# Optimization experiments

Measured on AMD Instinct MI355X. Metric: run time of the kernel, lower is better.

## Reference

```python
import jax, jax.numpy as jnp
import numpy as np

B, S, L = 2, 2048, 2048
H, KVH, D = 16, 4, 128
HID = H * D
EPS = 1e-6
SCALE = 1.0 / np.sqrt(D)


def rmsnorm(x, w, eps=EPS):
    # normalize over last dim (head_size), fp32 math
    xf = x.astype(jnp.float32)
    var = jnp.mean(xf * xf, axis=-1, keepdims=True)
    return (xf * jax.lax.rsqrt(var + eps)).astype(x.dtype) * w


def setup_inputs() -> dict:
    key = jax.random.key(0)
    ks = jax.random.split(key, 5)
    s = 1.0 / np.sqrt(HID)
    return {
        "x": jax.random.normal(ks[0], (B, S, HID), jnp.float32),
        "c": jax.random.normal(ks[1], (B, L, HID), jnp.float32),
        "wq": jax.random.normal(ks[2], (HID, H * D), jnp.float32) * s,
        "wkv": jax.random.normal(ks[3], (HID, KVH * D * 2), jnp.float32) * s,
        "wo": jax.random.normal(ks[4], (H * D, HID), jnp.float32) * s,
        "norm_q_w": jnp.ones((D,), jnp.float32),
        "norm_k_w": jnp.ones((D,), jnp.float32),
    }


def reference(x, c, wq, wkv, wo, norm_q_w, norm_k_w):
    bs, seq_len, _ = x.shape
    c_len = c.shape[1]
    n_rep = H // KVH
    # Q projection + per-head RMSNorm
    xq = (x @ wq).reshape(bs, seq_len, H, D)
    xq = rmsnorm(xq, norm_q_w)
    # packed KV projection: view(..., kvh, hd, 2), unbind last dim
    ckv = (c @ wkv).reshape(bs, c_len, KVH, D, 2)
    ck, cv = ckv[..., 0], ckv[..., 1]
    ck = rmsnorm(ck, norm_k_w)
    # GQA repeat_kv (repeat_interleave over head dim)
    ck = jnp.repeat(ck, n_rep, axis=2)  # [b, L, H, D]
    cv = jnp.repeat(cv, n_rep, axis=2)
    # SDPA cross-attention, softmax in fp32
    scores = jnp.einsum("bqhd,bkhd->bhqk", xq, ck) * SCALE
    attn = jax.nn.softmax(scores.astype(jnp.float32), axis=-1).astype(xq.dtype)
    out = jnp.einsum("bhqk,bkhd->bqhd", attn, cv)
    out = out.reshape(bs, seq_len, H * D)
    return out @ wo
```

## Files before the change

### kernel.cpp

```cpp
#include <hip/hip_runtime.h>

#define B_ 2
#define S_ 2048
#define L_ 2048
#define H_ 16
#define KVH_ 4
#define D_ 128
#define HID_ 2048
#define EPS_ 1e-6f

typedef unsigned short u16;
typedef unsigned int u32;
typedef __bf16 bf16x8 __attribute__((ext_vector_type(8)));
typedef float f32x4 __attribute__((ext_vector_type(4)));
typedef unsigned u32x2v __attribute__((ext_vector_type(2)));
typedef unsigned u32x4v __attribute__((ext_vector_type(4)));

__device__ __forceinline__ float bf2f(u32 u) {
  union { u32 i; float f; } x; x.i = u << 16; return x.f;
}
__device__ __forceinline__ u16 f2bf(float f) {
  union { float f; u32 i; } x; x.f = f;
  return (u16)((x.i + 0x7fffu + ((x.i >> 16) & 1u)) >> 16);
}
__device__ __forceinline__ u32 pack_bf16(float a, float b) {
#if __has_builtin(__builtin_amdgcn_cvt_pk_bf16_f32)
  typedef __bf16 bf16x2 __attribute__((ext_vector_type(2)));
  union { bf16x2 v; u32 u; } c;
  c.v = __builtin_amdgcn_cvt_pk_bf16_f32(a, b);
  return c.u;
#else
  return (u32)f2bf(a) | ((u32)f2bf(b) << 16);
#endif
}
__device__ __forceinline__ void gl2lds16(const u16* g, u16* l) {
  __builtin_amdgcn_global_load_lds(
      (const __attribute__((address_space(1))) u32*)g,
      (__attribute__((address_space(3))) u32*)l, 16, 0, 0);
}

#if __has_builtin(__builtin_amdgcn_permlane32_swap) && __has_builtin(__builtin_amdgcn_permlane16_swap)
#define HAS_PLS 1
#else
#define HAS_PLS 0
#endif

__device__ __forceinline__ u32x4v ctoa(u32 xa, u32 xb, u32 ya, u32 yb,
                                       int quad, int l15) {
  u32x4v f;
#if HAS_PLS
  u32x2v t1 = __builtin_amdgcn_permlane32_swap(xa, ya, false, false);
  u32x2v t2 = __builtin_amdgcn_permlane16_swap(t1.x, t1.y, false, false);
  u32x2v t3 = __builtin_amdgcn_permlane32_swap(xb, yb, false, false);
  u32x2v t4 = __builtin_amdgcn_permlane16_swap(t3.x, t3.y, false, false);
  f.x = t2.x; f.y = t4.x; f.z = t2.y; f.w = t4.y;
#else
  int a0 = (((2 * quad) & 3) * 16 + l15) << 2;
  int a1 = (((2 * quad + 1) & 3) * 16 + l15) << 2;
  u32 xa0 = __builtin_amdgcn_ds_bpermute(a0, xa), ya0 = __builtin_amdgcn_ds_bpermute(a0, ya);
  u32 xb0 = __builtin_amdgcn_ds_bpermute(a0, xb), yb0 = __builtin_amdgcn_ds_bpermute(a0, yb);
  u32 xa1 = __builtin_amdgcn_ds_bpermute(a1, xa), ya1 = __builtin_amdgcn_ds_bpermute(a1, ya);
  u32 xb1 = __builtin_amdgcn_ds_bpermute(a1, xb), yb1 = __builtin_amdgcn_ds_bpermute(a1, yb);
  bool hi = quad >= 2;
  f.x = hi ? ya0 : xa0; f.y = hi ? yb0 : xb0;
  f.z = hi ? ya1 : xa1; f.w = hi ? yb1 : xb1;
#endif
  return f;
}

__global__ __launch_bounds__(256) void cvt_bf16(const float* __restrict__ in,
                                                u16* __restrict__ out, int n4) {
  int i = blockIdx.x * 256 + threadIdx.x;
  if (i >= n4) return;
  float4 v = ((const float4*)in)[i];
  uint2 o;
  o.x = pack_bf16(v.x, v.y);
  o.y = pack_bf16(v.z, v.w);
  ((uint2*)out)[i] = o;
}

__global__ __launch_bounds__(256) void transp_bf16(const float* __restrict__ A,
                                                   u16* __restrict__ At, int R, int C) {
  __shared__ float t[64][65];
  int c0 = blockIdx.x * 64, r0 = blockIdx.y * 64;
  int tx = threadIdx.x & 63, ty = threadIdx.x >> 6;
  for (int i = ty; i < 64; i += 4)
    t[i][tx] = A[(size_t)(r0 + i) * C + c0 + tx];
  __syncthreads();
  for (int i = ty; i < 64; i += 4)
    At[(size_t)(c0 + i) * R + r0 + tx] = f2bf(t[tx][i]);
}

__device__ __forceinline__ void store_out(u16* p, float v) { *p = f2bf(v); }
__device__ __forceinline__ void store_out(float* p, float v) { *p = v; }

template <typename OutT>
__global__ __launch_bounds__(256, 2) void gemm_bt(const u16* __restrict__ A,
                                                  const u16* __restrict__ Bt,
                                                  OutT* __restrict__ C,
                                                  int M, int N, int K) {
  __shared__ u16 sA[128 * 32];
  __shared__ u16 sB[128 * 32];
  const int tid = threadIdx.x;
  const int wave = tid >> 6, lane = tid & 63;
  const int quad = lane >> 4, l15 = lane & 15;
  const int m0 = blockIdx.x * 128, n0 = blockIdx.y * 128;
  const int wm = (wave >> 1) * 64, wn = (wave & 1) * 64;
  const u16* aP = A + (size_t)m0 * K;
  const u16* bP = Bt + (size_t)n0 * K;
  const int sr = lane >> 2;
  const int sc = (lane & 3) * 8;
  const int r0 = wave * 32, r1 = wave * 32 + 16;

  f32x4 acc[4][4];
  for (int i = 0; i < 4; i++)
    for (int j = 0; j < 4; j++)
      for (int r = 0; r < 4; r++) acc[i][j][r] = 0.0f;

  for (int k0 = 0; k0 < K; k0 += 32) {
    gl2lds16(aP + (size_t)(r0 + sr) * K + k0 + sc, &sA[r0 * 32]);
    gl2lds16(aP + (size_t)(r1 + sr) * K + k0 + sc, &sA[r1 * 32]);
    gl2lds16(bP + (size_t)(r0 + sr) * K + k0 + sc, &sB[r0 * 32]);
    gl2lds16(bP + (size_t)(r1 + sr) * K + k0 + sc, &sB[r1 * 32]);
    __syncthreads();
    bf16x8 afrag[4], bfrag[4];
    for (int i = 0; i < 4; i++)
      afrag[i] = *(const bf16x8*)&sA[(wm + i * 16 + l15) * 32 + quad * 8];
    for (int j = 0; j < 4; j++)
      bfrag[j] = *(const bf16x8*)&sB[(wn + j * 16 + l15) * 32 + quad * 8];
    for (int i = 0; i < 4; i++)
      for (int j = 0; j < 4; j++)
        acc[i][j] = __builtin_amdgcn_mfma_f32_16x16x32_bf16(afrag[i], bfrag[j], acc[i][j], 0, 0, 0);
    __syncthreads();
  }
  for (int i = 0; i < 4; i++)
    for (int j = 0; j < 4; j++) {
      int row = m0 + wm + i * 16 + quad * 4;
      int col = n0 + wn + j * 16 + l15;
      for (int r = 0; r < 4; r++)
        store_out(&C[(size_t)(row + r) * N + col], acc[i][j][r]);
    }
}

__global__ __launch_bounds__(256) void knorm_deint(const u16* __restrict__ CKV,
                                                   const float* __restrict__ w,
                                                   u16* __restrict__ K,
                                                   u16* __restrict__ Vt) {
  __shared__ u16 vbuf[128][66];
  const int tid = threadIdx.x, wave = tid >> 6, lane = tid & 63;
  const int l0 = blockIdx.x * 64, kvh = blockIdx.y, b = blockIdx.z;
  for (int it = 0; it < 16; it++) {
    int ll = wave * 16 + it;
    int row = b * L_ + l0 + ll;
    const u16* src = CKV + (size_t)row * 1024 + kvh * 256;
    u32 p0 = *(const u32*)&src[lane * 2];
    u32 p1 = *(const u32*)&src[(lane + 64) * 2];
    float k0 = bf2f(p0 & 0xffff), v0 = bf2f(p0 >> 16);
    float k1 = bf2f(p1 & 0xffff), v1 = bf2f(p1 >> 16);
    float ss = k0 * k0 + k1 * k1;
    for (int off = 1; off < 64; off <<= 1) ss += __shfl_xor(ss, off);
    float sc = rsqrtf(ss * (1.0f / 128.0f) + EPS_);
    size_t kb = (((size_t)b * KVH_ + kvh) * L_ + l0 + ll) * D_;
    K[kb + lane] = f2bf(k0 * sc * w[lane]);
    K[kb + lane + 64] = f2bf(k1 * sc * w[lane + 64]);
    vbuf[lane][ll] = f2bf(v0);
    vbuf[lane + 64][ll] = f2bf(v1);
  }
  __syncthreads();
  for (int it = tid; it < 128 * 32; it += 256) {
    int d = it >> 5, cc = (it & 31) * 2;
    u32 pk = (u32)vbuf[d][cc] | ((u32)vbuf[d][cc + 1] << 16);
    *(u32*)&Vt[(((size_t)b * KVH_ + kvh) * D_ + d) * L_ + l0 + cc] = pk;
  }
}

__global__ __launch_bounds__(256, 2) void attn(const u16* __restrict__ XQ,
                                               const float* __restrict__ nw,
                                               const u16* __restrict__ K,
                                               const u16* __restrict__ Vt,
                                               u16* __restrict__ AO) {
  __shared__ u16 sk[4][128 * 32];
  __shared__ u16 sv[4][128 * 32];
  const int tid = threadIdx.x, wave = tid >> 6, lane = tid & 63;
  const int quad = lane >> 4, l15 = lane & 15;
  const int qt = blockIdx.x, h = blockIdx.y, b = blockIdx.z;
  const int kvh = h >> 2;
  const int s0 = qt * 128, wr0 = wave * 32;

  bf16x8 qf[2][4];
  {
    const float cexp = 0.12753102331322172f;
    const u16* qrow = XQ + (size_t)(b * S_ + s0 + wr0 + l15) * HID_ + h * D_;
    for (int i = 0; i < 2; i++) {
      const u16* qr = qrow + (size_t)i * 16 * HID_;
      float vals[4][8];
      float ss = 0.0f;
      for (int kc = 0; kc < 4; kc++) {
        uint4 u = *(const uint4*)&qr[kc * 32 + quad * 8];
        u32 uu[4] = {u.x, u.y, u.z, u.w};
        for (int e = 0; e < 4; e++) {
          float lo = bf2f(uu[e] & 0xffff), hi = bf2f(uu[e] >> 16);
          vals[kc][2 * e] = lo;
          vals[kc][2 * e + 1] = hi;
          ss += lo * lo + hi * hi;
        }
      }
      ss += __shfl_xor(ss, 16);
      ss += __shfl_xor(ss, 32);
      float scale = rsqrtf(ss * (1.0f / 128.0f) + EPS_) * cexp;
      for (int kc = 0; kc < 4; kc++) {
        float4 w0 = *(const float4*)&nw[kc * 32 + quad * 8];
        float4 w1 = *(const float4*)&nw[kc * 32 + quad * 8 + 4];
        union { u32x4v u; bf16x8 v; } q;
        q.u.x = pack_bf16(vals[kc][0] * scale * w0.x, vals[kc][1] * scale * w0.y);
        q.u.y = pack_bf16(vals[kc][2] * scale * w0.z, vals[kc][3] * scale * w0.w);
        q.u.z = pack_bf16(vals[kc][4] * scale * w1.x, vals[kc][5] * scale * w1.y);
        q.u.w = pack_bf16(vals[kc][6] * scale * w1.z, vals[kc][7] * scale * w1.w);
        qf[i][kc] = q.v;
      }
    }
  }

  float psum[2] = {0.0f, 0.0f};
  f32x4 o[2][8];
  for (int i = 0; i < 2; i++)
    for (int n = 0; n < 8; n++)
      for (int r = 0; r < 4; r++) o[i][n][r] = 0.0f;

  const u16* kbase = K + ((size_t)(b * KVH_ + kvh) * L_) * D_;
  const u16* vbase = Vt + ((size_t)(b * KVH_ + kvh) * D_) * L_;
  const int srow = lane >> 2;
  const int scol = ((lane & 3) ^ ((lane >> 3) & 3)) * 8;
  const int swq = (quad ^ ((l15 >> 1) & 3)) * 8;

  for (int l0 = 0; l0 < L_; l0 += 128) {
    const u16* kb = kbase + (size_t)l0 * D_ + wave * 32;
    for (int is = 0; is < 8; is++)
      gl2lds16(kb + (size_t)(is * 16 + srow) * D_ + scol, &sk[wave][is * 16 * 32]);
    const u16* vb = vbase + l0 + wave * 32;
    for (int is = 0; is < 8; is++)
      gl2lds16(vb + (size_t)(is * 16 + srow) * L_ + scol, &sv[wave][is * 16 * 32]);
    __syncthreads();

    for (int cc = 0; cc < 4; cc++) {
      f32x4 sacc[2][2];
      for (int jj = 0; jj < 2; jj++)
        for (int i = 0; i < 2; i++)
          for (int r = 0; r < 4; r++) sacc[jj][i][r] = 0.0f;
      for (int jj = 0; jj < 2; jj++) {
        int j = cc * 2 + jj;
        for (int kc = 0; kc < 4; kc++) {
          bf16x8 kf = *(const bf16x8*)&sk[kc][(j * 16 + l15) * 32 + swq];
          for (int i = 0; i < 2; i++)
            sacc[jj][i] = __builtin_amdgcn_mfma_f32_16x16x32_bf16(kf, qf[i][kc], sacc[jj][i], 0, 0, 0);
        }
      }
      union { u32x4v u; bf16x8 v; } pf[2];
      for (int i = 0; i < 2; i++) {
        float p0[4], p1[4];
        for (int r = 0; r < 4; r++) {
          p0[r] = exp2f(sacc[0][i][r]);
          p1[r] = exp2f(sacc[1][i][r]);
          psum[i] += p0[r] + p1[r];
        }
        u32 xa = pack_bf16(p0[0], p0[1]), xb = pack_bf16(p0[2], p0[3]);
        u32 ya = pack_bf16(p1[0], p1[1]), yb = pack_bf16(p1[2], p1[3]);
        pf[i].u = ctoa(xa, xb, ya, yb, quad, l15);
      }
      for (int n = 0; n < 8; n++) {
        bf16x8 vf = *(const bf16x8*)&sv[cc][(n * 16 + l15) * 32 + swq];
        for (int i = 0; i < 2; i++)
          o[i][n] = __builtin_amdgcn_mfma_f32_16x16x32_bf16(pf[i].v, vf, o[i][n], 0, 0, 0);
      }
    }
    __syncthreads();
  }

  for (int i = 0; i < 2; i++) {
    float s = psum[i];
    s += __shfl_xor(s, 16);
    s += __shfl_xor(s, 32);
    float linv = 1.0f / s;
    float lr[4];
    for (int r = 0; r < 4; r++) lr[r] = __shfl(linv, quad * 4 + r);
    u16* ob = AO + (size_t)(b * S_ + s0 + wr0 + i * 16) * HID_ + h * D_;
    for (int n = 0; n < 8; n++)
      for (int r = 0; r < 4; r++)
        ob[(size_t)(quad * 4 + r) * HID_ + n * 16 + l15] = f2bf(o[i][n][r] * lr[r]);
  }
}

extern "C" void kernel_launch(void* const* d_in, const int* in_sizes, int n_in,
                              void* d_out, int out_size, void* d_ws, size_t ws_size,
                              hipStream_t stream) {
  const float* x = (const float*)d_in[0];
  const float* c = (const float*)d_in[1];
  const float* wq = (const float*)d_in[2];
  const float* wkv = (const float*)d_in[3];
  const float* wo = (const float*)d_in[4];
  const float* nqw = (const float*)d_in[5];
  const float* nkw = (const float*)d_in[6];
  float* out = (float*)d_out;

  const int M = B_ * S_;
  char* p = (char*)d_ws;
  auto alloc = [&](size_t bytes) {
    char* r = p;
    p += (bytes + 255) & ~(size_t)255;
    return r;
  };
  u16* xbf = (u16*)alloc((size_t)M * HID_ * 2);
  u16* cbf = (u16*)alloc((size_t)M * HID_ * 2);
  u16* wqT = (u16*)alloc((size_t)HID_ * HID_ * 2);
  u16* wkvT = (u16*)alloc((size_t)1024 * HID_ * 2);
  u16* woT = (u16*)alloc((size_t)HID_ * HID_ * 2);
  u16* XQ = (u16*)alloc((size_t)M * HID_ * 2);
  u16* CKV = (u16*)alloc((size_t)M * 1024 * 2);
  u16* Kb = (u16*)alloc((size_t)B_ * KVH_ * L_ * D_ * 2);
  u16* Vt = (u16*)alloc((size_t)B_ * KVH_ * D_ * L_ * 2);
  u16* AO = (u16*)alloc((size_t)M * HID_ * 2);

  cvt_bf16<<<8192, 256, 0, stream>>>(x, xbf, M * HID_ / 4);
  cvt_bf16<<<8192, 256, 0, stream>>>(c, cbf, M * HID_ / 4);
  transp_bf16<<<dim3(32, 32), 256, 0, stream>>>(wq, wqT, HID_, HID_);
  transp_bf16<<<dim3(16, 32), 256, 0, stream>>>(wkv, wkvT, HID_, 1024);
  transp_bf16<<<dim3(32, 32), 256, 0, stream>>>(wo, woT, HID_, HID_);
  gemm_bt<u16><<<dim3(32, 16), 256, 0, stream>>>(xbf, wqT, XQ, M, HID_, HID_);
  gemm_bt<u16><<<dim3(32, 8), 256, 0, stream>>>(cbf, wkvT, CKV, M, 1024, HID_);
  knorm_deint<<<dim3(32, 4, 2), 256, 0, stream>>>(CKV, nkw, Kb, Vt);
  attn<<<dim3(16, 16, 2), 256, 0, stream>>>(XQ, nqw, Kb, Vt, AO);
  gemm_bt<float><<<dim3(32, 16), 256, 0, stream>>>(AO, woT, out, M, HID_, HID_);
}
```

Baseline: 405.1 us.

## Double-buffer K/V tiles in attention loop with prefetch and wave priority

Splits the key dimension into 64-wide tiles held in two LDS buffers, so the load of the next K/V tile is issued before computing on the current one, with a partial vmcnt wait and a raw barrier. It also raises wave priority around the MFMA blocks and swaps exp2f for the hardware exp2 builtin. The aim is to hide global-to-LDS latency, which the old loop exposed behind a full syncthreads. In exchange it runs twice as many loop iterations and barriers, and correctness depends on the hand-written waitcnt count matching the eight loads per stage.

```diff
diff --git a/kernel.cpp b/kernel.cpp
--- a/kernel.cpp
+++ b/kernel.cpp
@@ -31,6 +31,13 @@
   return c.u;
 #else
   return (u32)f2bf(a) | ((u32)f2bf(b) << 16);
+#endif
+}
+__device__ __forceinline__ float fexp2(float x) {
+#if __has_builtin(__builtin_amdgcn_exp2f)
+  return __builtin_amdgcn_exp2f(x);
+#else
+  return exp2f(x);
 #endif
 }
 __device__ __forceinline__ void gl2lds16(const u16* g, u16* l) {
@@ -179,13 +186,30 @@
                                                const u16* __restrict__ K,
                                                const u16* __restrict__ Vt,
                                                u16* __restrict__ AO) {
-  __shared__ u16 sk[4][128 * 32];
-  __shared__ u16 sv[4][128 * 32];
+  __shared__ u16 sk[2][4][64 * 32];
+  __shared__ u16 sv[2][2][128 * 32];
   const int tid = threadIdx.x, wave = tid >> 6, lane = tid & 63;
   const int quad = lane >> 4, l15 = lane & 15;
   const int qt = blockIdx.x, h = blockIdx.y, b = blockIdx.z;
   const int kvh = h >> 2;
   const int s0 = qt * 128, wr0 = wave * 32;
+
+  const u16* kbase = K + ((size_t)(b * KVH_ + kvh) * L_) * D_;
+  const u16* vbase = Vt + ((size_t)(b * KVH_ + kvh) * D_) * L_;
+  const int srow = lane >> 2;
+  const int scol = ((lane & 3) ^ ((lane >> 3) & 3)) * 8;
+  const int swq = (quad ^ ((l15 >> 1) & 3)) * 8;
+  const int vc = wave >> 1, vd0 = (wave & 1) * 64;
+
+  auto stage = [&](int l0, int buf) {
+    const u16* kb = kbase + (size_t)l0 * D_ + wave * 32;
+    for (int is = 0; is < 4; is++)
+      gl2lds16(kb + (size_t)(is * 16 + srow) * D_ + scol, &sk[buf][wave][is * 16 * 32]);
+    const u16* vb = vbase + l0 + vc * 32;
+    for (int is = 0; is < 4; is++)
+      gl2lds16(vb + (size_t)(vd0 + is * 16 + srow) * L_ + scol,
+               &sv[buf][vc][(vd0 + is * 16) * 32]);
+  };
 
   bf16x8 qf[2][4];
   {
@@ -227,53 +251,54 @@
     for (int n = 0; n < 8; n++)
       for (int r = 0; r < 4; r++) o[i][n][r] = 0.0f;
 
-  const u16* kbase = K + ((size_t)(b * KVH_ + kvh) * L_) * D_;
-  const u16* vbase = Vt + ((size_t)(b * KVH_ + kvh) * D_) * L_;
-  const int srow = lane >> 2;
-  const int scol = ((lane & 3) ^ ((lane >> 3) & 3)) * 8;
-  const int swq = (quad ^ ((l15 >> 1) & 3)) * 8;
-
-  for (int l0 = 0; l0 < L_; l0 += 128) {
-    const u16* kb = kbase + (size_t)l0 * D_ + wave * 32;
-    for (int is = 0; is < 8; is++)
-      gl2lds16(kb + (size_t)(is * 16 + srow) * D_ + scol, &sk[wave][is * 16 * 32]);
-    const u16* vb = vbase + l0 + wave * 32;
-    for (int is = 0; is < 8; is++)
-      gl2lds16(vb + (size_t)(is * 16 + srow) * L_ + scol, &sv[wave][is * 16 * 32]);
-    __syncthreads();
-
-    for (int cc = 0; cc < 4; cc++) {
+  stage(0, 0);
+  int cur = 0;
+  const int NT = L_ / 64;
+  for (int t = 0; t < NT; t++) {
+    if (t + 1 < NT) {
+      stage((t + 1) * 64, cur ^ 1);
+      asm volatile("s_waitcnt vmcnt(8)\n\ts_barrier" ::: "memory");
+    } else {
+      asm volatile("s_waitcnt vmcnt(0)\n\ts_barrier" ::: "memory");
+    }
+
+    for (int cc = 0; cc < 2; cc++) {
       f32x4 sacc[2][2];
       for (int jj = 0; jj < 2; jj++)
         for (int i = 0; i < 2; i++)
           for (int r = 0; r < 4; r++) sacc[jj][i][r] = 0.0f;
+      __builtin_amdgcn_s_setprio(1);
       for (int jj = 0; jj < 2; jj++) {
         int j = cc * 2 + jj;
         for (int kc = 0; kc < 4; kc++) {
-          bf16x8 kf = *(const bf16x8*)&sk[kc][(j * 16 + l15) * 32 + swq];
+          bf16x8 kf = *(const bf16x8*)&sk[cur][kc][(j * 16 + l15) * 32 + swq];
           for (int i = 0; i < 2; i++)
             sacc[jj][i] = __builtin_amdgcn_mfma_f32_16x16x32_bf16(kf, qf[i][kc], sacc[jj][i], 0, 0, 0);
         }
       }
+      __builtin_amdgcn_s_setprio(0);
       union { u32x4v u; bf16x8 v; } pf[2];
       for (int i = 0; i < 2; i++) {
         float p0[4], p1[4];
         for (int r = 0; r < 4; r++) {
-          p0[r] = exp2f(sacc[0][i][r]);
-          p1[r] = exp2f(sacc[1][i][r]);
+          p0[r] = fexp2(sacc[0][i][r]);
+          p1[r] = fexp2(sacc[1][i][r]);
           psum[i] += p0[r] + p1[r];
         }
         u32 xa = pack_bf16(p0[0], p0[1]), xb = pack_bf16(p0[2], p0[3]);
         u32 ya = pack_bf16(p1[0], p1[1]), yb = pack_bf16(p1[2], p1[3]);
         pf[i].u = ctoa(xa, xb, ya, yb, quad, l15);
       }
+      __builtin_amdgcn_s_setprio(1);
       for (int n = 0; n < 8; n++) {
-        bf16x8 vf = *(const bf16x8*)&sv[cc][(n * 16 + l15) * 32 + swq];
+        bf16x8 vf = *(const bf16x8*)&sv[cur][cc][(n * 16 + l15) * 32 + swq];
         for (int i = 0; i < 2; i++)
           o[i][n] = __builtin_amdgcn_mfma_f32_16x16x32_bf16(pf[i].v, vf, o[i][n], 0, 0, 0);
       }
+      __builtin_amdgcn_s_setprio(0);
     }
-    __syncthreads();
+    asm volatile("s_barrier" ::: "memory");
+    cur ^= 1;
   }
 
   for (int i = 0; i < 2; i++) {
```

After: 387.9 us. -4.2%, faster.
